# Kernel optimization log

Measured on AMD Instinct MI355X. Metric: run time of the kernel, lower is better.

The kernel has to match this reference:

```python
import jax, jax.numpy as jnp
from jax import lax
import numpy as np

NPOINT = 1024   # S: number of sampled centroids
NSAMPLE = 32    # K: neighbors per centroid (unmasked ball query = k-nearest via argsort)


def _gather(p, i):
    # p: [B,N,C], i: [B,...] int -> [B,...,C]
    return jax.vmap(lambda pb, ib: pb[ib])(p, i)


def _fps(xyz, farthest_init, npoint):
    # Iterative farthest point sampling, faithful to the torch loop.
    B, N, _ = xyz.shape
    dist0 = jnp.full((B, N), 1e10, dtype=xyz.dtype)

    def step(carry, _):
        distance, farthest = carry
        centroid = jnp.take_along_axis(xyz, farthest[:, None, None], axis=1)  # [B,1,3]
        d = jnp.sum((xyz - centroid) ** 2, -1)          # [B,N]
        distance = jnp.minimum(distance, d)
        return (distance, jnp.argmax(distance, -1)), farthest

    _, cent = lax.scan(step, (dist0, farthest_init.astype(jnp.int32)), None, length=npoint)
    return cent.T  # [B, npoint]


def _sq_dist(src, dst):
    # src: [B,S,3], dst: [B,N,3] -> [B,S,N]
    return (jnp.sum(src ** 2, -1)[:, :, None]
            + jnp.sum(dst ** 2, -1)[:, None, :]
            - 2.0 * jnp.einsum('bsc,bnc->bsn', src, dst))


def setup_inputs() -> dict:
    key = jax.random.key(0)
    ks = jax.random.split(key, 6)
    B, N, C = 8, 4096, 6
    inp = {
        'xyz': jax.random.normal(ks[0], (B, N, 3), jnp.float32),
        'points': jax.random.normal(ks[1], (B, N, C), jnp.float32),
        'farthest_init': jax.random.randint(ks[2], (B,), 0, N),
    }
    dims = [C + 3, 64, 64, 128]
    for li in range(3):
        inp[f'w{li}'] = jax.random.normal(ks[3 + li], (dims[li + 1], dims[li]), jnp.float32) * 0.1
        inp[f'b{li}'] = jnp.zeros((dims[li + 1],), jnp.float32)
    return inp


def reference(xyz, points, farthest_init, w0, b0, w1, b1, w2, b2):
    fps_idx = _fps(xyz, farthest_init, NPOINT)            # [B,S]
    new_xyz = _gather(xyz, fps_idx)                       # [B,S,3]
    dist = _sq_dist(new_xyz, xyz)                         # [B,S,N]
    _, idx = lax.top_k(-dist, NSAMPLE)                    # k-nearest == argsort[:, :, :K]
    g_xyz = _gather(xyz, idx) - new_xyz[:, :, None, :]    # [B,S,K,3]
    g_pts = _gather(points, idx)                          # [B,S,K,C]
    h = jnp.concatenate([g_xyz, g_pts], axis=-1)          # [B,S,K,C+3]
    for w, b in ((w0, b0), (w1, b1), (w2, b2)):           # 1x1 conv MLP + relu
        h = jax.nn.relu(jnp.einsum('bskc,oc->bsko', h, w) + b)
    new_points = jnp.max(h, axis=2)                       # max-pool over K -> [B,S,128]
    return new_xyz, new_points
```

## Files before the change

### kernel.cpp

```cpp
#include <hip/hip_runtime.h>

#define INF_F 3.402823466e+38f
typedef unsigned long long u64;
typedef __attribute__((ext_vector_type(2))) float f32x2;

__device__ __forceinline__ float f_add(float a, float b){ return __fadd_rn(a,b); }
__device__ __forceinline__ float f_sub(float a, float b){ return __fsub_rn(a,b); }
__device__ __forceinline__ float f_mul(float a, float b){ return __fmul_rn(a,b); }

__device__ __forceinline__ f32x2 pk_add(f32x2 a, f32x2 b){ f32x2 d; asm("v_pk_add_f32 %0, %1, %2" : "=v"(d) : "v"(a), "v"(b)); return d; }
__device__ __forceinline__ f32x2 pk_mul(f32x2 a, f32x2 b){ f32x2 d; asm("v_pk_mul_f32 %0, %1, %2" : "=v"(d) : "v"(a), "v"(b)); return d; }

template<int CTRL>
__device__ __forceinline__ double dpp_d(double x) {
    u64 u = (u64)__double_as_longlong(x);
    int lo = __builtin_amdgcn_update_dpp(0, (int)(unsigned)u,        CTRL, 0xF, 0xF, true);
    int hi = __builtin_amdgcn_update_dpp(0, (int)(unsigned)(u>>32), CTRL, 0xF, 0xF, true);
    return __longlong_as_double((long long)(((u64)(unsigned)hi << 32) | (unsigned)lo));
}
template<int CTRL>
__device__ __forceinline__ float dpp_f(float x) {
    int r = __builtin_amdgcn_update_dpp(0, __float_as_int(x), CTRL, 0xF, 0xF, true);
    return __int_as_float(r);
}
__device__ __forceinline__ double swz16_d(double x) {
    u64 u = (u64)__double_as_longlong(x);
    int lo = __builtin_amdgcn_ds_swizzle((int)(unsigned)u,        0x401F);
    int hi = __builtin_amdgcn_ds_swizzle((int)(unsigned)(u>>32), 0x401F);
    return __longlong_as_double((long long)(((u64)(unsigned)hi << 32) | (unsigned)lo));
}
__device__ __forceinline__ float swz16_f(float x) {
    return __int_as_float(__builtin_amdgcn_ds_swizzle(__float_as_int(x), 0x401F));
}
__device__ __forceinline__ double readlane_d(double x, int l) {
    u64 u = (u64)__double_as_longlong(x);
    int lo = __builtin_amdgcn_readlane((int)(unsigned)u,        l);
    int hi = __builtin_amdgcn_readlane((int)(unsigned)(u>>32), l);
    return __longlong_as_double((long long)(((u64)(unsigned)hi << 32) | (unsigned)lo));
}
__device__ __forceinline__ double pack_key(float nd, unsigned low) {
    return __longlong_as_double((long long)(((u64)__float_as_uint(nd) << 32) | (u64)low));
}

__global__ __launch_bounds__(256, 1) void fps_kernel(
    const float* __restrict__ xyz, const int* __restrict__ farthest_init,
    float* __restrict__ out_new_xyz)
{
    const int b    = blockIdx.x;
    const int tid  = threadIdx.x;
    const int lane = tid & 63;
    const int wid  = tid >> 6;

    __shared__ float  sx[4096], sy[4096], sz[4096];
    __shared__ int    hist[1024];
    __shared__ double red[2][4];

    const float* xb = xyz + (size_t)b * 4096 * 3;
    for (int n = tid; n < 4096; n += 256) {
        sx[n] = xb[n*3+0]; sy[n] = xb[n*3+1]; sz[n] = xb[n*3+2];
    }
    __syncthreads();

    f32x2 px[8], py[8], pz[8], dist2[8];
    #pragma unroll
    for (int jp = 0; jp < 8; ++jp) {
        const int n0 = (2*jp) * 256 + tid, n1 = n0 + 256;
        px[jp] = (f32x2){sx[n0], sx[n1]};
        py[jp] = (f32x2){sy[n0], sy[n1]};
        pz[jp] = (f32x2){sz[n0], sz[n1]};
        dist2[jp] = (f32x2){1e10f, 1e10f};
    }
    const unsigned lowbase = 4095u - (unsigned)tid;

    int far = farthest_init[b];
    int p = 0;
    #pragma unroll 1
    for (int it = 0; it < 1024; ++it) {
        if (tid == 0) hist[it] = far;
        const float cx = sx[far], cy = sy[far], cz = sz[far];
        const f32x2 ncx = (f32x2){-cx, -cx};
        const f32x2 ncy = (f32x2){-cy, -cy};
        const f32x2 ncz = (f32x2){-cz, -cz};

        double a0 = -1.0, a1 = -1.0, a2 = -1.0, a3 = -1.0;
        #pragma unroll
        for (int jp = 0; jp < 8; ++jp) {
            f32x2 dx = pk_add(px[jp], ncx);
            f32x2 dy = pk_add(py[jp], ncy);
            f32x2 dz = pk_add(pz[jp], ncz);
            f32x2 d2 = pk_add(pk_add(pk_mul(dx,dx), pk_mul(dy,dy)), pk_mul(dz,dz));
            float nd0 = fminf(dist2[jp][0], d2[0]); dist2[jp][0] = nd0;
            float nd1 = fminf(dist2[jp][1], d2[1]); dist2[jp][1] = nd1;
            double k0 = pack_key(nd0, lowbase - (unsigned)((2*jp)*256));
            double k1 = pack_key(nd1, lowbase - (unsigned)((2*jp+1)*256));
            if (jp & 1) { a2 = fmax(a2, k0); a3 = fmax(a3, k1); }
            else        { a0 = fmax(a0, k0); a1 = fmax(a1, k1); }
        }
        double best = fmax(fmax(a0, a1), fmax(a2, a3));
        best = fmax(best, dpp_d<0xB1>(best));
        best = fmax(best, dpp_d<0x4E>(best));
        best = fmax(best, dpp_d<0x141>(best));
        best = fmax(best, dpp_d<0x140>(best));
        best = fmax(best, swz16_d(best));
        double wb = fmax(readlane_d(best, 0), readlane_d(best, 32));
        if (lane == 0) red[p][wid] = wb;
        __syncthreads();
        double g = fmax(fmax(red[p][0], red[p][1]), fmax(red[p][2], red[p][3]));
        far = 4095 - (int)(unsigned)((u64)__double_as_longlong(g) & 0xFFFFFFFFull);
        p ^= 1;
    }
    __syncthreads();
    #pragma unroll
    for (int q = 0; q < 4; ++q) {
        int s  = q * 256 + tid;
        int id = hist[s];
        float* o = out_new_xyz + ((size_t)b * 1024 + s) * 3;
        o[0] = sx[id]; o[1] = sy[id]; o[2] = sz[id];
    }
}

template<int G>
__device__ __forceinline__ double rebuild8(const double (&key)[64], double w) {
    const double DINF = __builtin_huge_val();
    double m = DINF;
    #pragma unroll
    for (int e = 0; e < 8; ++e) {
        double v = key[G*8+e];
        v = (v > w) ? v : DINF;
        m = fmin(m, v);
    }
    return m;
}

__global__ __launch_bounds__(256, 1) void knn_kernel(
    const float* __restrict__ xyz, const float* __restrict__ new_xyz,
    int* __restrict__ out_idx)
{
    const int tid  = threadIdx.x;
    const int lane = tid & 63;
    const int wid  = tid >> 6;
    const int blk  = blockIdx.x * 4 + wid;
    const int b    = blk >> 10;
    const double DINF = __builtin_huge_val();

    const float* xb = xyz + (size_t)b * 4096 * 3;
    const float* cp = new_xyz + (size_t)blk * 3;
    const float cx = cp[0], cy = cp[1], cz = cp[2];
    const float src2 = f_add(f_add(f_mul(cx,cx), f_mul(cy,cy)), f_mul(cz,cz));

    double key[64];
    #pragma unroll
    for (int j = 0; j < 64; ++j) {
        const int n = j * 64 + lane;
        const float* pt = xb + n * 3;
        float x = pt[0], y = pt[1], z = pt[2];
        float dst2 = f_add(f_add(f_mul(x,x), f_mul(y,y)), f_mul(z,z));
        float dot  = f_add(f_add(f_mul(cx,x), f_mul(cy,y)), f_mul(cz,z));
        float d = f_sub(f_add(src2, dst2), f_mul(2.0f, dot));
        key[j] = __longlong_as_double((long long)(((u64)__float_as_uint(d) << 32) | (u64)(unsigned)n));
    }

    double gm[8];
    #pragma unroll
    for (int g = 0; g < 8; ++g) {
        double m = key[g*8];
        #pragma unroll
        for (int e = 1; e < 8; ++e) m = fmin(m, key[g*8+e]);
        gm[g] = m;
    }

    double w = -1.0;
    int myidx = 0;
    #pragma unroll 1
    for (int t = 0; t < 32; ++t) {
        double lm = fmin(fmin(fmin(gm[0], gm[1]), fmin(gm[2], gm[3])),
                         fmin(fmin(gm[4], gm[5]), fmin(gm[6], gm[7])));
        lm = fmin(lm, dpp_d<0xB1>(lm));
        lm = fmin(lm, dpp_d<0x4E>(lm));
        lm = fmin(lm, dpp_d<0x141>(lm));
        lm = fmin(lm, dpp_d<0x140>(lm));
        lm = fmin(lm, swz16_d(lm));
        double gmin = fmin(readlane_d(lm, 0), readlane_d(lm, 32));
        int n = (int)(unsigned)((u64)__double_as_longlong(gmin) & 0xFFFFFFFFull);
        if (lane == t) myidx = n;
        w = gmin;
        const int gs = __builtin_amdgcn_readfirstlane(n >> 9);
        switch (gs) {
            case 0: gm[0] = rebuild8<0>(key, w); break;
            case 1: gm[1] = rebuild8<1>(key, w); break;
            case 2: gm[2] = rebuild8<2>(key, w); break;
            case 3: gm[3] = rebuild8<3>(key, w); break;
            case 4: gm[4] = rebuild8<4>(key, w); break;
            case 5: gm[5] = rebuild8<5>(key, w); break;
            case 6: gm[6] = rebuild8<6>(key, w); break;
            case 7: gm[7] = rebuild8<7>(key, w); break;
        }
    }
    if (lane < 32) out_idx[(size_t)blk * 32 + lane] = myidx;
}

__global__ __launch_bounds__(256, 1) void mlp_kernel(
    const float* __restrict__ xyz, const float* __restrict__ points,
    const int* __restrict__ knn_idx,
    const float* __restrict__ w0, const float* __restrict__ b0,
    const float* __restrict__ w1, const float* __restrict__ b1,
    const float* __restrict__ w2, const float* __restrict__ b2,
    const float* __restrict__ new_xyz, float* __restrict__ out_np)
{
    const int tid = threadIdx.x;
    const int k   = tid & 31;
    const int gs  = blockIdx.x * 8 + (tid >> 5);
    const int b   = gs >> 10;
    const int n   = knn_idx[(size_t)gs * 32 + k];

    const float cx = new_xyz[gs*3+0], cy = new_xyz[gs*3+1], cz = new_xyz[gs*3+2];
    const float* pxyz = xyz + ((size_t)b * 4096 + n) * 3;
    float h0[9];
    h0[0] = pxyz[0] - cx;
    h0[1] = pxyz[1] - cy;
    h0[2] = pxyz[2] - cz;
    const float* pp = points + ((size_t)b * 4096 + n) * 6;
    #pragma unroll
    for (int c = 0; c < 6; ++c) h0[3 + c] = pp[c];

    float h1[64];
    #pragma unroll
    for (int o = 0; o < 64; ++o) {
        float acc = b0[o];
        #pragma unroll
        for (int c = 0; c < 9; ++c) acc = fmaf(h0[c], w0[o*9+c], acc);
        h1[o] = fmaxf(acc, 0.0f);
    }

    float h2[64];
    #pragma unroll
    for (int o = 0; o < 64; ++o) {
        float acc = b1[o];
        #pragma unroll
        for (int c = 0; c < 64; ++c) acc = fmaf(h1[c], w1[o*64+c], acc);
        h2[o] = fmaxf(acc, 0.0f);
    }

    float* outp = out_np + (size_t)gs * 128;
    for (int og = 0; og < 4; ++og) {
        float keep = 0.0f;
        for (int o2 = 0; o2 < 32; ++o2) {
            const int o = og * 32 + o2;
            float acc = b2[o];
            #pragma unroll
            for (int c = 0; c < 64; ++c) acc = fmaf(h2[c], w2[o*64+c], acc);
            float m = fmaxf(acc, 0.0f);
            m = fmaxf(m, dpp_f<0xB1>(m));
            m = fmaxf(m, dpp_f<0x4E>(m));
            m = fmaxf(m, dpp_f<0x141>(m));
            m = fmaxf(m, dpp_f<0x140>(m));
            m = fmaxf(m, swz16_f(m));
            keep = (k == o2) ? m : keep;
        }
        outp[og * 32 + k] = keep;
    }
}

__global__ __launch_bounds__(256) void knn_mlp_kernel(
    const float* __restrict__ xyz, const float* __restrict__ points,
    const float* __restrict__ w0, const float* __restrict__ b0,
    const float* __restrict__ w1, const float* __restrict__ b1,
    const float* __restrict__ w2, const float* __restrict__ b2,
    const float* __restrict__ new_xyz, float* __restrict__ out_np)
{
    const int blk    = blockIdx.x;
    const int b      = blk >> 7;
    const int s_base = (blk & 127) * 8;
    const int tid    = threadIdx.x;
    const int lane   = tid & 63;
    const int wid    = tid >> 6;

    __shared__ float sx[4096], sy[4096], sz[4096];
    __shared__ float cent[8][3];
    __shared__ int   idxbuf[8][32];

    const float* xb = xyz + (size_t)b * 4096 * 3;
    for (int n = tid; n < 4096; n += 256) {
        sx[n] = xb[n*3+0]; sy[n] = xb[n*3+1]; sz[n] = xb[n*3+2];
    }
    if (tid < 24) ((float*)cent)[tid] = new_xyz[((size_t)b * 1024 + s_base) * 3 + tid];
    __syncthreads();

    for (int si = 0; si < 2; ++si) {
        const int sl = wid * 2 + si;
        const float cx = cent[sl][0], cy = cent[sl][1], cz = cent[sl][2];
        const float src2 = f_add(f_add(f_mul(cx,cx), f_mul(cy,cy)), f_mul(cz,cz));
        float d[64];
        #pragma unroll
        for (int j = 0; j < 64; ++j) {
            int n = j * 64 + lane;
            float x = sx[n], y = sy[n], z = sz[n];
            float dst2 = f_add(f_add(f_mul(x,x), f_mul(y,y)), f_mul(z,z));
            float dot  = f_add(f_add(f_mul(cx,x), f_mul(cy,y)), f_mul(cz,z));
            d[j] = f_sub(f_add(src2, dst2), f_mul(2.0f, dot));
        }
        int myg  = 0;
        int prev = -1;
        for (int t = 0; t < 32; ++t) {
            float bv = INF_F; int bi = 0x7fffffff;
            #pragma unroll
            for (int j = 0; j < 64; ++j) {
                int n = j * 64 + lane;
                if (n == prev) d[j] = INF_F;
                float v = d[j];
                if (v < bv) { bv = v; bi = n; }
            }
            #pragma unroll
            for (int m = 1; m < 64; m <<= 1) {
                float ov = __shfl_xor(bv, m);
                int   oi = __shfl_xor(bi, m);
                if (ov < bv || (ov == bv && oi < bi)) { bv = ov; bi = oi; }
            }
            if (lane == t) myg = bi;
            prev = bi;
        }
        if (lane < 32) idxbuf[sl][lane] = myg;
    }
    __syncthreads();

    const int k   = tid & 31;
    const int sl2 = tid >> 5;
    const int s   = s_base + sl2;
    const int n   = idxbuf[sl2][k];

    const float cx = cent[sl2][0], cy = cent[sl2][1], cz = cent[sl2][2];
    float h0[9];
    h0[0] = sx[n] - cx;
    h0[1] = sy[n] - cy;
    h0[2] = sz[n] - cz;
    const float* pp = points + ((size_t)b * 4096 + n) * 6;
    #pragma unroll
    for (int c = 0; c < 6; ++c) h0[3 + c] = pp[c];

    float h1[64];
    #pragma unroll
    for (int o = 0; o < 64; ++o) {
        float acc = b0[o];
        #pragma unroll
        for (int c = 0; c < 9; ++c) acc = fmaf(h0[c], w0[o*9+c], acc);
        h1[o] = fmaxf(acc, 0.0f);
    }
    float h2[64];
    #pragma unroll
    for (int o = 0; o < 64; ++o) {
        float acc = b1[o];
        #pragma unroll
        for (int c = 0; c < 64; ++c) acc = fmaf(h1[c], w1[o*64+c], acc);
        h2[o] = fmaxf(acc, 0.0f);
    }
    float* outp = out_np + ((size_t)b * 1024 + s) * 128;
    for (int og = 0; og < 4; ++og) {
        float keep = 0.0f;
        for (int o2 = 0; o2 < 32; ++o2) {
            const int o = og * 32 + o2;
            float acc = b2[o];
            #pragma unroll
            for (int c = 0; c < 64; ++c) acc = fmaf(h2[c], w2[o*64+c], acc);
            float m = fmaxf(acc, 0.0f);
            #pragma unroll
            for (int mm = 1; mm < 32; mm <<= 1)
                m = fmaxf(m, __shfl_xor(m, mm));
            keep = (k == o2) ? m : keep;
        }
        outp[og * 32 + k] = keep;
    }
}

extern "C" void kernel_launch(void* const* d_in, const int* in_sizes, int n_in,
                              void* d_out, int out_size, void* d_ws, size_t ws_size,
                              hipStream_t stream) {
    const float* xyz           = (const float*)d_in[0];
    const float* points        = (const float*)d_in[1];
    const int*   farthest_init = (const int*)  d_in[2];
    const float* w0 = (const float*)d_in[3];
    const float* b0 = (const float*)d_in[4];
    const float* w1 = (const float*)d_in[5];
    const float* b1 = (const float*)d_in[6];
    const float* w2 = (const float*)d_in[7];
    const float* b2 = (const float*)d_in[8];

    float* out        = (float*)d_out;
    float* new_xyz    = out;
    float* new_points = out + 8 * 1024 * 3;

    fps_kernel<<<8, 256, 0, stream>>>(xyz, farthest_init, new_xyz);

    if (ws_size >= (size_t)(8192 * 32 * sizeof(int))) {
        int* knn_idx = (int*)d_ws;
        knn_kernel<<<2048, 256, 0, stream>>>(xyz, new_xyz, knn_idx);
        mlp_kernel<<<1024, 256, 0, stream>>>(xyz, points, knn_idx,
                                             w0, b0, w1, b1, w2, b2,
                                             new_xyz, new_points);
    } else {
        knn_mlp_kernel<<<1024, 256, 0, stream>>>(xyz, points, w0, b0, w1, b1, w2, b2,
                                                 new_xyz, new_points);
    }
}
```

Before: 772.4 us.

## Pack FPS points as float4, use readlane wave reductions, packed-FMA MLP

FPS now stores each point as a float4 in shared memory, so one vector LDS read fetches a centroid, and it prefetches the next centroid right after the reduction. The wave max/min reductions drop the ds_swizzle step and instead combine four readlanes (lanes 0, 16, 32, 48), which avoids an LDS-path swizzle inside the serial loop. The MLP layers 2 and 3 switch to v_pk_fma_f32 over pairs of input channels, which halves the FMA instruction count but splits each dot product into two partial sums added at the end. The KNN kernel reuses the new reduction. The risks are extra readlane scalar traffic, and small rounding differences from the reordered accumulation.

```diff
diff --git a/kernel.cpp b/kernel.cpp
--- a/kernel.cpp
+++ b/kernel.cpp
@@ -10,6 +10,7 @@
 
 __device__ __forceinline__ f32x2 pk_add(f32x2 a, f32x2 b){ f32x2 d; asm("v_pk_add_f32 %0, %1, %2" : "=v"(d) : "v"(a), "v"(b)); return d; }
 __device__ __forceinline__ f32x2 pk_mul(f32x2 a, f32x2 b){ f32x2 d; asm("v_pk_mul_f32 %0, %1, %2" : "=v"(d) : "v"(a), "v"(b)); return d; }
+__device__ __forceinline__ f32x2 pk_fma(f32x2 a, f32x2 b, f32x2 c){ f32x2 d; asm("v_pk_fma_f32 %0, %1, %2, %3" : "=v"(d) : "v"(a), "v"(b), "v"(c)); return d; }
 
 template<int CTRL>
 __device__ __forceinline__ double dpp_d(double x) {
@@ -23,12 +24,6 @@
     int r = __builtin_amdgcn_update_dpp(0, __float_as_int(x), CTRL, 0xF, 0xF, true);
     return __int_as_float(r);
 }
-__device__ __forceinline__ double swz16_d(double x) {
-    u64 u = (u64)__double_as_longlong(x);
-    int lo = __builtin_amdgcn_ds_swizzle((int)(unsigned)u,        0x401F);
-    int hi = __builtin_amdgcn_ds_swizzle((int)(unsigned)(u>>32), 0x401F);
-    return __longlong_as_double((long long)(((u64)(unsigned)hi << 32) | (unsigned)lo));
-}
 __device__ __forceinline__ float swz16_f(float x) {
     return __int_as_float(__builtin_amdgcn_ds_swizzle(__float_as_int(x), 0x401F));
 }
@@ -40,6 +35,25 @@
 }
 __device__ __forceinline__ double pack_key(float nd, unsigned low) {
     return __longlong_as_double((long long)(((u64)__float_as_uint(nd) << 32) | (u64)low));
+}
+
+__device__ __forceinline__ double wave_max_key(double k) {
+    k = fmax(k, dpp_d<0xB1>(k));
+    k = fmax(k, dpp_d<0x4E>(k));
+    k = fmax(k, dpp_d<0x141>(k));
+    k = fmax(k, dpp_d<0x140>(k));
+    double a = readlane_d(k, 0),  b = readlane_d(k, 16);
+    double c = readlane_d(k, 32), d = readlane_d(k, 48);
+    return fmax(fmax(a, b), fmax(c, d));
+}
+__device__ __forceinline__ double wave_min_key(double k) {
+    k = fmin(k, dpp_d<0xB1>(k));
+    k = fmin(k, dpp_d<0x4E>(k));
+    k = fmin(k, dpp_d<0x141>(k));
+    k = fmin(k, dpp_d<0x140>(k));
+    double a = readlane_d(k, 0),  b = readlane_d(k, 16);
+    double c = readlane_d(k, 32), d = readlane_d(k, 48);
+    return fmin(fmin(a, b), fmin(c, d));
 }
 
 __global__ __launch_bounds__(256, 1) void fps_kernel(
@@ -51,33 +65,34 @@
     const int lane = tid & 63;
     const int wid  = tid >> 6;
 
-    __shared__ float  sx[4096], sy[4096], sz[4096];
+    __shared__ float4 sp[4096];
     __shared__ int    hist[1024];
     __shared__ double red[2][4];
 
     const float* xb = xyz + (size_t)b * 4096 * 3;
-    for (int n = tid; n < 4096; n += 256) {
-        sx[n] = xb[n*3+0]; sy[n] = xb[n*3+1]; sz[n] = xb[n*3+2];
-    }
+    for (int n = tid; n < 4096; n += 256)
+        sp[n] = make_float4(xb[n*3+0], xb[n*3+1], xb[n*3+2], 0.0f);
     __syncthreads();
 
     f32x2 px[8], py[8], pz[8], dist2[8];
     #pragma unroll
     for (int jp = 0; jp < 8; ++jp) {
         const int n0 = (2*jp) * 256 + tid, n1 = n0 + 256;
-        px[jp] = (f32x2){sx[n0], sx[n1]};
-        py[jp] = (f32x2){sy[n0], sy[n1]};
-        pz[jp] = (f32x2){sz[n0], sz[n1]};
+        float4 a = sp[n0], c = sp[n1];
+        px[jp] = (f32x2){a.x, c.x};
+        py[jp] = (f32x2){a.y, c.y};
+        pz[jp] = (f32x2){a.z, c.z};
         dist2[jp] = (f32x2){1e10f, 1e10f};
     }
     const unsigned lowbase = 4095u - (unsigned)tid;
 
     int far = farthest_init[b];
+    float4 cen = sp[far];
+    float cx = cen.x, cy = cen.y, cz = cen.z;
     int p = 0;
     #pragma unroll 1
     for (int it = 0; it < 1024; ++it) {
         if (tid == 0) hist[it] = far;
-        const float cx = sx[far], cy = sy[far], cz = sz[far];
         const f32x2 ncx = (f32x2){-cx, -cx};
         const f32x2 ncy = (f32x2){-cy, -cy};
         const f32x2 ncz = (f32x2){-cz, -cz};
@@ -96,26 +111,23 @@
             if (jp & 1) { a2 = fmax(a2, k0); a3 = fmax(a3, k1); }
             else        { a0 = fmax(a0, k0); a1 = fmax(a1, k1); }
         }
-        double best = fmax(fmax(a0, a1), fmax(a2, a3));
-        best = fmax(best, dpp_d<0xB1>(best));
-        best = fmax(best, dpp_d<0x4E>(best));
-        best = fmax(best, dpp_d<0x141>(best));
-        best = fmax(best, dpp_d<0x140>(best));
-        best = fmax(best, swz16_d(best));
-        double wb = fmax(readlane_d(best, 0), readlane_d(best, 32));
-        if (lane == 0) red[p][wid] = wb;
+        double wkey = wave_max_key(fmax(fmax(a0, a1), fmax(a2, a3)));
+        if (lane == 0) red[p][wid] = wkey;
         __syncthreads();
-        double g = fmax(fmax(red[p][0], red[p][1]), fmax(red[p][2], red[p][3]));
+        const double g = fmax(fmax(red[p][0], red[p][1]),
+                              fmax(red[p][2], red[p][3]));
         far = 4095 - (int)(unsigned)((u64)__double_as_longlong(g) & 0xFFFFFFFFull);
+        float4 cc = sp[far];
+        cx = cc.x; cy = cc.y; cz = cc.z;
         p ^= 1;
     }
     __syncthreads();
     #pragma unroll
     for (int q = 0; q < 4; ++q) {
         int s  = q * 256 + tid;
-        int id = hist[s];
+        float4 cc = sp[hist[s]];
         float* o = out_new_xyz + ((size_t)b * 1024 + s) * 3;
-        o[0] = sx[id]; o[1] = sy[id]; o[2] = sz[id];
+        o[0] = cc.x; o[1] = cc.y; o[2] = cc.z;
     }
 }
 
@@ -141,7 +153,6 @@
     const int wid  = tid >> 6;
     const int blk  = blockIdx.x * 4 + wid;
     const int b    = blk >> 10;
-    const double DINF = __builtin_huge_val();
 
     const float* xb = xyz + (size_t)b * 4096 * 3;
     const float* cp = new_xyz + (size_t)blk * 3;
@@ -175,12 +186,7 @@
     for (int t = 0; t < 32; ++t) {
         double lm = fmin(fmin(fmin(gm[0], gm[1]), fmin(gm[2], gm[3])),
                          fmin(fmin(gm[4], gm[5]), fmin(gm[6], gm[7])));
-        lm = fmin(lm, dpp_d<0xB1>(lm));
-        lm = fmin(lm, dpp_d<0x4E>(lm));
-        lm = fmin(lm, dpp_d<0x141>(lm));
-        lm = fmin(lm, dpp_d<0x140>(lm));
-        lm = fmin(lm, swz16_d(lm));
-        double gmin = fmin(readlane_d(lm, 0), readlane_d(lm, 32));
+        double gmin = wave_min_key(lm);
         int n = (int)(unsigned)((u64)__double_as_longlong(gmin) & 0xFFFFFFFFull);
         if (lane == t) myidx = n;
         w = gmin;
@@ -223,33 +229,42 @@
     #pragma unroll
     for (int c = 0; c < 6; ++c) h0[3 + c] = pp[c];
 
-    float h1[64];
-    #pragma unroll
-    for (int o = 0; o < 64; ++o) {
-        float acc = b0[o];
-        #pragma unroll
-        for (int c = 0; c < 9; ++c) acc = fmaf(h0[c], w0[o*9+c], acc);
-        h1[o] = fmaxf(acc, 0.0f);
-    }
-
-    float h2[64];
-    #pragma unroll
-    for (int o = 0; o < 64; ++o) {
-        float acc = b1[o];
-        #pragma unroll
-        for (int c = 0; c < 64; ++c) acc = fmaf(h1[c], w1[o*64+c], acc);
-        h2[o] = fmaxf(acc, 0.0f);
-    }
-
+    f32x2 h1p[32];
+    #pragma unroll
+    for (int o = 0; o < 64; o += 2) {
+        float accA = b0[o], accB = b0[o+1];
+        #pragma unroll
+        for (int c = 0; c < 9; ++c) {
+            accA = fmaf(h0[c], w0[o*9+c],     accA);
+            accB = fmaf(h0[c], w0[(o+1)*9+c], accB);
+        }
+        h1p[o>>1] = (f32x2){fmaxf(accA, 0.0f), fmaxf(accB, 0.0f)};
+    }
+
+    const f32x2* w1v = (const f32x2*)w1;
+    f32x2 h2p[32];
+    #pragma unroll
+    for (int o = 0; o < 64; o += 2) {
+        f32x2 accA = (f32x2){b1[o],   0.0f};
+        f32x2 accB = (f32x2){b1[o+1], 0.0f};
+        #pragma unroll
+        for (int i = 0; i < 32; ++i) {
+            accA = pk_fma(h1p[i], w1v[o*32+i],     accA);
+            accB = pk_fma(h1p[i], w1v[(o+1)*32+i], accB);
+        }
+        h2p[o>>1] = (f32x2){fmaxf(accA[0]+accA[1], 0.0f), fmaxf(accB[0]+accB[1], 0.0f)};
+    }
+
+    const f32x2* w2v = (const f32x2*)w2;
     float* outp = out_np + (size_t)gs * 128;
     for (int og = 0; og < 4; ++og) {
         float keep = 0.0f;
         for (int o2 = 0; o2 < 32; ++o2) {
             const int o = og * 32 + o2;
-            float acc = b2[o];
+            f32x2 acc = (f32x2){b2[o], 0.0f};
             #pragma unroll
-            for (int c = 0; c < 64; ++c) acc = fmaf(h2[c], w2[o*64+c], acc);
-            float m = fmaxf(acc, 0.0f);
+            for (int i = 0; i < 32; ++i) acc = pk_fma(h2p[i], w2v[o*32+i], acc);
+            float m = fmaxf(acc[0] + acc[1], 0.0f);
             m = fmaxf(m, dpp_f<0xB1>(m));
             m = fmaxf(m, dpp_f<0x4E>(m));
             m = fmaxf(m, dpp_f<0x141>(m));
```

Measured after the change: 781.0 us. Within noise of the previous version (+1.1%).
